# Optimization experiments

Measured on AMD Instinct MI355X. Metric: run time of the kernel, lower is better.

Reference implementation:

```python
import jax, jax.numpy as jnp
import numpy as np

DIM = 128
HEADS = 4
DIM_HEAD = 32
N_EMBD = HEADS * DIM_HEAD  # 128
SCALE = DIM_HEAD ** -0.5


def conv2d(x, w, b):
    # NCHW conv, 3x3, stride 1, SAME padding (= padding=1 in torch)
    out = jax.lax.conv_general_dilated(
        x, w, window_strides=(1, 1), padding='SAME',
        dimension_numbers=('NCHW', 'OIHW', 'NCHW'))
    return out + b[None, :, None, None]


def conv_block(x, w1, b1, w2, b2):
    # Conv -> ReLU -> Conv (the to_q/to_k/to_v pattern)
    return conv2d(jax.nn.relu(conv2d(x, w1, b1)), w2, b2)


def setup_inputs() -> dict:
    key = jax.random.key(0)
    ks = jax.random.split(key, 20)
    B, C, S = 4, DIM, 32
    H, W = 128, 512
    wscale = 0.05

    def cw(k, cout, cin):
        return jax.random.normal(k, (cout, cin, 3, 3), jnp.float32) * wscale

    inp = {
        'x': jax.random.normal(ks[0], (B, C, S, S), jnp.float32),
        'y': jax.random.normal(ks[1], (B, C, H, W), jnp.float32),
        'u': jax.random.randint(ks[2], (B, S, S), 0, W),
        'q_w1': cw(ks[3], N_EMBD, DIM), 'q_b1': jnp.zeros((N_EMBD,), jnp.float32),
        'q_w2': cw(ks[4], N_EMBD, N_EMBD), 'q_b2': jnp.zeros((N_EMBD,), jnp.float32),
        'k_w1': cw(ks[5], N_EMBD, DIM), 'k_b1': jnp.zeros((N_EMBD,), jnp.float32),
        'k_w2': cw(ks[6], N_EMBD, N_EMBD), 'k_b2': jnp.zeros((N_EMBD,), jnp.float32),
        'v_w1': cw(ks[7], N_EMBD, DIM), 'v_b1': jnp.zeros((N_EMBD,), jnp.float32),
        'v_w2': cw(ks[8], N_EMBD, N_EMBD), 'v_b2': jnp.zeros((N_EMBD,), jnp.float32),
        'proj_w': cw(ks[9], DIM, N_EMBD), 'proj_b': jnp.zeros((DIM,), jnp.float32),
    }
    return inp


def reference(x, y, u, q_w1, q_b1, q_w2, q_b2, k_w1, k_b1, k_w2, k_b2,
              v_w1, v_b1, v_w2, v_b2, proj_w, proj_b):
    B, C, S, _ = x.shape
    _, _, H, W = y.shape
    SS = S * S

    # Q from the (B,C,S,S) query grid -> (B, S^2, n_embd)
    q = conv_block(x, q_w1, q_b1, q_w2, q_b2).reshape(B, N_EMBD, SS).transpose(0, 2, 1)

    # K, V from the (B,C,H,W) map
    k = conv_block(y, k_w1, k_b1, k_w2, k_b2)  # (B, E, H, W)
    v = conv_block(y, v_w1, v_b1, v_w2, v_b2)

    # Gather columns of K/V along W per query index u (clamped)
    uc = jnp.clip(u, 0, W - 1).astype(jnp.int32).reshape(B, 1, 1, SS)
    ks = jnp.take_along_axis(k, uc, axis=3).transpose(0, 3, 2, 1)  # (B, SS, H, E)
    vs = jnp.take_along_axis(v, uc, axis=3).transpose(0, 3, 2, 1)  # (B, SS, H, E)

    # Per-query attention over the H axis
    dot = SCALE * jnp.einsum('bqe,bqhe->bqh', q, ks)  # (B, SS, H)
    attn = jax.nn.softmax(dot, axis=-1)
    a = jnp.einsum('bqh,bqhe->bqe', attn, vs)  # (B, SS, E)

    a = a.transpose(0, 2, 1).reshape(B, N_EMBD, S, S)
    z = jax.nn.relu(conv2d(a, proj_w, proj_b))  # (B, DIM, S, S)
    return z
```

## Files before the change

kernel.cpp:

```cpp
#include <hip/hip_runtime.h>
#include <stdint.h>

typedef __attribute__((ext_vector_type(16))) float f32x16;
typedef __attribute__((ext_vector_type(8))) short s16x8;

#define WAITVM(n) asm volatile("s_waitcnt vmcnt(" #n ")" ::: "memory")
#define WAITLGKM0 asm volatile("s_waitcnt lgkmcnt(0)" ::: "memory")

__device__ inline short bf16b(float f) {
  uint32_t x = __float_as_uint(f);
  return (short)((x + 0x7fffu + ((x >> 16) & 1u)) >> 16);
}
__device__ inline float bfu(uint16_t u) { return __uint_as_float(((uint32_t)u) << 16); }

__device__ inline void gll16(const void* g, void* l) {
  __builtin_amdgcn_global_load_lds((const __attribute__((address_space(1))) void*)g,
                                   (__attribute__((address_space(3))) void*)l, 16, 0, 0);
}

__global__ __launch_bounds__(256) void packw_k(
    const float* w0, const float* w1, const float* w2, const float* w3,
    const float* w4, const float* w5, const float* w6, s16x8* dst) {
  const float* srcs[7] = {w0, w1, w2, w3, w4, w5, w6};
  const int widx = blockIdx.y;
  const float* src = srcs[widx];
  const int gid = blockIdx.x * 256 + threadIdx.x;
  const int lane = gid & 63, frag = gid >> 6;
  const int nblk = frag & 3, ks = (frag >> 2) & 1, chunk = (frag >> 3) & 3, tap = frag >> 5;
  const int co = nblk * 32 + (lane & 31);
  const int cib = chunk * 32 + ks * 16 + (lane >> 5) * 8;
  s16x8 v;
#pragma unroll
  for (int j = 0; j < 8; ++j)
    v[j] = bf16b(src[((size_t)co * 128 + cib + j) * 9 + tap]);
  dst[(size_t)widx * 18432 + (size_t)frag * 64 + lane] = v;
}

template <int TW>
__global__ __launch_bounds__(256) void nchw2nhwc_k(
    const float* __restrict__ in, uint16_t* __restrict__ out, int H, int W) {
  __shared__ float tile[128][TW + 1];
  const int b = blockIdx.z, h = blockIdx.y, w0 = blockIdx.x * TW;
  for (int idx = threadIdx.x; idx < 128 * TW; idx += 256) {
    int c = idx / TW, w = idx - c * TW;
    tile[c][w] = in[(((size_t)b * 128 + c) * H + h) * W + w0 + w];
  }
  __syncthreads();
  for (int idx = threadIdx.x; idx < TW * 16; idx += 256) {
    int w = idx >> 4, cg = idx & 15;
    s16x8 v;
#pragma unroll
    for (int j = 0; j < 8; ++j) v[j] = bf16b(tile[cg * 8 + j][w]);
    *reinterpret_cast<s16x8*>(out + ((((size_t)b * H + h) * W + w0 + w) << 7) + cg * 8) = v;
  }
}

template <int OMODE, bool RELU, typename Tout>
__global__ __launch_bounds__(256, 3) void convmf7_k(
    const uint16_t* __restrict__ in, const s16x8* __restrict__ wpk,
    const float* __restrict__ bias, Tout* __restrict__ out,
    const uint16_t* __restrict__ zp, int H, int W) {
  constexpr int CP = 34, RP = 6, RPCP = RP * CP;
  constexpr int SLOTS = 4 * RPCP;
  constexpr int SPT = 4;
  __shared__ s16x8 lds[2][SPT * 256];
  const int b = blockIdx.z, r0 = blockIdx.y * 4, c0 = blockIdx.x * 32;
  const int tid = threadIdx.x, lane = tid & 63, wn = tid >> 6;
  const int wbase = tid & 192;

  const uint16_t* gsrc[SPT];
#pragma unroll
  for (int i = 0; i < SPT; ++i) {
    const int s = tid + i * 256;
    const int kq = s / RPCP;
    const int rem = s - kq * RPCP;
    const int r = rem / CP, c = rem - r * CP;
    const int gr = r0 + r - 1, gc = c0 + c - 1;
    const bool ok = (s < SLOTS) && gr >= 0 && gr < H && gc >= 0 && gc < W;
    gsrc[i] = ok ? (in + (((size_t)b * H + gr) * W + gc) * 128 + kq * 8) : zp;
  }

  const s16x8* __restrict__ wbl = wpk + wn * 64 + lane;
  s16x8 wf[9];
#pragma unroll
  for (int t = 0; t < 9; ++t) wf[t] = wbl[t * 2048];

#pragma unroll
  for (int i = 0; i < SPT; ++i) gll16(gsrc[i], &lds[0][wbase + i * 256]);

  f32x16 acc[4];
#pragma unroll
  for (int i = 0; i < 4; ++i)
#pragma unroll
    for (int r = 0; r < 16; ++r) acc[i][r] = 0.f;

  const int abase = (lane >> 5) * RPCP + (lane & 31);
  WAITVM(0);
  __builtin_amdgcn_s_barrier();
  __builtin_amdgcn_sched_barrier(0);

#pragma unroll
  for (int chunk = 0; chunk < 4; ++chunk) {
    const int cb = chunk & 1;
    const s16x8* __restrict__ Lb = &lds[cb][abase];
#pragma unroll
    for (int p = 0; p < 6; ++p) {
      const int ks = p / 3, kx = p - ks * 3;
      s16x8 ar[6];
#pragma unroll
      for (int r = 0; r < 6; ++r) ar[r] = Lb[ks * 2 * RPCP + r * CP + kx];
      if (chunk < 3 && p < SPT)
        gll16(gsrc[p] + (chunk + 1) * 32, &lds[cb ^ 1][wbase + p * 256]);
      __builtin_amdgcn_sched_barrier(0);
      __builtin_amdgcn_s_barrier();
      WAITLGKM0;
      __builtin_amdgcn_sched_barrier(0);
      __builtin_amdgcn_s_setprio(1);
#pragma unroll
      for (int ky = 0; ky < 3; ++ky) {
#pragma unroll
        for (int mf = 0; mf < 4; ++mf)
          acc[mf] = __builtin_amdgcn_mfma_f32_32x32x16_bf16(ar[mf + ky], wf[ky * 3 + kx],
                                                            acc[mf], 0, 0, 0);
      }
      __builtin_amdgcn_s_setprio(0);
      if (!(chunk == 3 && ks == 1)) {
        const int nc = (ks == 0) ? chunk : chunk + 1;
        const int nks = (ks == 0) ? 1 : 0;
#pragma unroll
        for (int ky = 0; ky < 3; ++ky) {
          const int tap = ky * 3 + kx;
          wf[tap] = wbl[((tap * 4 + nc) * 2 + nks) * 256];
        }
      }
      __builtin_amdgcn_sched_barrier(0);
      if (p == 5 && chunk < 3) WAITVM(9);
      __builtin_amdgcn_s_barrier();
    }
  }

  const int co = wn * 32 + (lane & 31);
  const float bv = bias[co];
#pragma unroll
  for (int mf = 0; mf < 4; ++mf) {
    const int gr = r0 + mf;
#pragma unroll
    for (int reg = 0; reg < 16; ++reg) {
      const int gc = c0 + (reg & 3) + 8 * (reg >> 2) + 4 * (lane >> 5);
      float v = acc[mf][reg] + bv;
      if (RELU) v = fmaxf(v, 0.f);
      size_t idx;
      if (OMODE == 0)      idx = (((size_t)b * H + gr) * W + gc) * 128 + co;
      else if (OMODE == 1) idx = (((size_t)b * W + gc) * H + gr) * 128 + co;
      else                 idx = (((size_t)b * 128 + co) * H + gr) * W + gc;
      if constexpr (sizeof(Tout) == 2) ((uint16_t*)out)[idx] = (uint16_t)bf16b(v);
      else out[idx] = v;
    }
  }
}

__global__ __launch_bounds__(128) void attn_dot_k(
    const float* __restrict__ qg, const uint16_t* __restrict__ Kg,
    const int* __restrict__ u, float* __restrict__ pout) {
  const int bs = blockIdx.x;
  const int b = bs >> 10;
  const int tid = threadIdx.x;
  __shared__ float sq[128];
  __shared__ float wred[2][2];
  sq[tid] = qg[(size_t)bs * 128 + tid];
  int w = u[bs]; w = w < 0 ? 0 : (w > 511 ? 511 : w);
  __syncthreads();
  const s16x8* kp = reinterpret_cast<const s16x8*>(
      Kg + (((size_t)b * 512 + w) * 128 + tid) * 128);
  float acc = 0.f;
#pragma unroll
  for (int i = 0; i < 16; ++i) {
    s16x8 v = kp[i];
#pragma unroll
    for (int j = 0; j < 8; ++j)
      acc = fmaf(sq[i * 8 + j], bfu((uint16_t)v[j]), acc);
  }
  const float d = acc * 0.17677669529663687f;
  float m = d;
#pragma unroll
  for (int o = 1; o < 64; o <<= 1) m = fmaxf(m, __shfl_xor(m, o));
  if ((tid & 63) == 0) wred[0][tid >> 6] = m;
  __syncthreads();
  m = fmaxf(wred[0][0], wred[0][1]);
  const float e = expf(d - m);
  float s = e;
#pragma unroll
  for (int o = 1; o < 64; o <<= 1) s += __shfl_xor(s, o);
  if ((tid & 63) == 0) wred[1][tid >> 6] = s;
  __syncthreads();
  s = wred[1][0] + wred[1][1];
  pout[(size_t)bs * 128 + tid] = e / s;
}

__global__ __launch_bounds__(128) void attn_pv_k(
    const float* __restrict__ pin, const uint16_t* __restrict__ Vg,
    const int* __restrict__ u, uint16_t* __restrict__ aout) {
  const int bs = blockIdx.x;
  const int b = bs >> 10;
  const int tid = threadIdx.x;
  const int eo = tid & 15, hg = tid >> 4;
  __shared__ float sp[128];
  __shared__ float red[8][128];
  sp[tid] = pin[(size_t)bs * 128 + tid];
  int w = u[bs]; w = w < 0 ? 0 : (w > 511 ? 511 : w);
  __syncthreads();
  const s16x8* vp = reinterpret_cast<const s16x8*>(
      Vg + ((size_t)b * 512 + w) * 16384) + eo;
  float a8[8];
#pragma unroll
  for (int j = 0; j < 8; ++j) a8[j] = 0.f;
#pragma unroll
  for (int hh = 0; hh < 16; ++hh) {
    const int h = hg * 16 + hh;
    s16x8 v = vp[h * 16];
    const float p = sp[h];
#pragma unroll
    for (int j = 0; j < 8; ++j) a8[j] = fmaf(p, bfu((uint16_t)v[j]), a8[j]);
  }
#pragma unroll
  for (int j = 0; j < 8; ++j) red[hg][eo * 8 + j] = a8[j];
  __syncthreads();
  float r = 0.f;
#pragma unroll
  for (int g = 0; g < 8; ++g) r += red[g][tid];
  aout[(size_t)bs * 128 + tid] = (uint16_t)bf16b(r);
}

extern "C" void kernel_launch(void* const* d_in, const int* in_sizes, int n_in,
                              void* d_out, int out_size, void* d_ws, size_t ws_size,
                              hipStream_t stream) {
  const float* x      = (const float*)d_in[0];
  const float* y      = (const float*)d_in[1];
  const int*   u      = (const int*)d_in[2];
  const float* q_w1   = (const float*)d_in[3];
  const float* q_b1   = (const float*)d_in[4];
  const float* q_w2   = (const float*)d_in[5];
  const float* q_b2   = (const float*)d_in[6];
  const float* k_w1   = (const float*)d_in[7];
  const float* k_b1   = (const float*)d_in[8];
  const float* k_w2   = (const float*)d_in[9];
  const float* k_b2   = (const float*)d_in[10];
  const float* v_w1   = (const float*)d_in[11];
  const float* v_b1   = (const float*)d_in[12];
  const float* v_w2   = (const float*)d_in[13];
  const float* v_b2   = (const float*)d_in[14];
  const float* proj_w = (const float*)d_in[15];
  const float* proj_b = (const float*)d_in[16];
  float* out = (float*)d_out;

  char* ws = (char*)d_ws;
  const size_t MB = 1 << 20;
  const size_t BIG = 64 * MB;
  const bool tierB = ws_size >= 203 * MB;
  uint16_t* A  = (uint16_t*)ws;
  uint16_t* Bb = (uint16_t*)(ws + BIG);
  uint16_t* KV = tierB ? (uint16_t*)(ws + 2 * BIG) : A;
  char* sm = ws + (tierB ? 3 : 2) * BIG;
  float*    qg  = (float*)sm;
  float*    pb  = (float*)(sm + 2 * MB);
  uint16_t* xbf = (uint16_t*)(sm + 4 * MB);
  uint16_t* t1  = (uint16_t*)(sm + 5 * MB);
  uint16_t* ab  = (uint16_t*)(sm + 6 * MB);
  s16x8*    wpk = (s16x8*)(sm + 7 * MB);
  uint16_t* zp  = (uint16_t*)(sm + 10 * MB);

  hipMemsetAsync(zp, 0, 1024, stream);
  packw_k<<<dim3(72, 7), 256, 0, stream>>>(q_w1, q_w2, k_w1, k_w2, v_w1, v_w2, proj_w, wpk);
  nchw2nhwc_k<32><<<dim3(1, 32, 4), 256, 0, stream>>>(x, xbf, 32, 32);
  nchw2nhwc_k<64><<<dim3(8, 128, 4), 256, 0, stream>>>(y, A, 128, 512);
  convmf7_k<0, true,  uint16_t><<<dim3(1, 8, 4), 256, 0, stream>>>(xbf, wpk + 0 * 18432, q_b1, t1, zp, 32, 32);
  convmf7_k<0, false, float   ><<<dim3(1, 8, 4), 256, 0, stream>>>(t1,  wpk + 1 * 18432, q_b2, qg, zp, 32, 32);
  convmf7_k<0, true,  uint16_t><<<dim3(16, 32, 4), 256, 0, stream>>>(A,  wpk + 2 * 18432, k_b1, Bb, zp, 128, 512);
  convmf7_k<1, false, uint16_t><<<dim3(16, 32, 4), 256, 0, stream>>>(Bb, wpk + 3 * 18432, k_b2, KV, zp, 128, 512);
  attn_dot_k<<<dim3(4096), 128, 0, stream>>>(qg, KV, u, pb);
  if (!tierB) nchw2nhwc_k<64><<<dim3(8, 128, 4), 256, 0, stream>>>(y, A, 128, 512);
  convmf7_k<0, true,  uint16_t><<<dim3(16, 32, 4), 256, 0, stream>>>(A,  wpk + 4 * 18432, v_b1, Bb, zp, 128, 512);
  convmf7_k<1, false, uint16_t><<<dim3(16, 32, 4), 256, 0, stream>>>(Bb, wpk + 5 * 18432, v_b2, KV, zp, 128, 512);
  attn_pv_k<<<dim3(4096), 128, 0, stream>>>(pb, KV, u, ab);
  convmf7_k<3, true, float><<<dim3(1, 8, 4), 256, 0, stream>>>(ab, wpk + 6 * 18432, proj_b, out, zp, 32, 32);
}
```

Measured before the change: 430.8 us.

## Fuse K and V first-layer convolutions into one dual-output MFMA kernel

Adds a conv kernel that loads each input tile of the y feature map into LDS once and computes both the K and V first 3x3 convs, with two accumulator sets and two weight register sets. This halves the input reads and LDS staging for the large first-layer convs and removes one kernel launch. The cost is doubled accumulator and weight register pressure (launch bounds 256,2), which may lower occupancy. It also needs a third big workspace buffer, so the non-fused path is kept for small workspaces.

```diff
diff --git a/kernel.cpp b/kernel.cpp
--- a/kernel.cpp
+++ b/kernel.cpp
@@ -155,6 +155,111 @@
       else                 idx = (((size_t)b * 128 + co) * H + gr) * W + gc;
       if constexpr (sizeof(Tout) == 2) ((uint16_t*)out)[idx] = (uint16_t)bf16b(v);
       else out[idx] = v;
+    }
+  }
+}
+
+__global__ __launch_bounds__(256, 2) void convmf7d_k(
+    const uint16_t* __restrict__ in, const s16x8* __restrict__ wpkK,
+    const s16x8* __restrict__ wpkV, const float* __restrict__ biasK,
+    const float* __restrict__ biasV, uint16_t* __restrict__ outK,
+    uint16_t* __restrict__ outV, const uint16_t* __restrict__ zp, int H, int W) {
+  constexpr int CP = 34, RP = 6, RPCP = RP * CP;
+  constexpr int SLOTS = 4 * RPCP;
+  constexpr int SPT = 4;
+  __shared__ s16x8 lds[2][SPT * 256];
+  const int b = blockIdx.z, r0 = blockIdx.y * 4, c0 = blockIdx.x * 32;
+  const int tid = threadIdx.x, lane = tid & 63, wn = tid >> 6;
+  const int wbase = tid & 192;
+
+  const uint16_t* gsrc[SPT];
+#pragma unroll
+  for (int i = 0; i < SPT; ++i) {
+    const int s = tid + i * 256;
+    const int kq = s / RPCP;
+    const int rem = s - kq * RPCP;
+    const int r = rem / CP, c = rem - r * CP;
+    const int gr = r0 + r - 1, gc = c0 + c - 1;
+    const bool ok = (s < SLOTS) && gr >= 0 && gr < H && gc >= 0 && gc < W;
+    gsrc[i] = ok ? (in + (((size_t)b * H + gr) * W + gc) * 128 + kq * 8) : zp;
+  }
+
+  const s16x8* __restrict__ wblK = wpkK + wn * 64 + lane;
+  const s16x8* __restrict__ wblV = wpkV + wn * 64 + lane;
+  s16x8 wfK[9], wfV[9];
+#pragma unroll
+  for (int t = 0; t < 9; ++t) { wfK[t] = wblK[t * 2048]; wfV[t] = wblV[t * 2048]; }
+
+#pragma unroll
+  for (int i = 0; i < SPT; ++i) gll16(gsrc[i], &lds[0][wbase + i * 256]);
+
+  f32x16 accK[4], accV[4];
+#pragma unroll
+  for (int i = 0; i < 4; ++i)
+#pragma unroll
+    for (int r = 0; r < 16; ++r) { accK[i][r] = 0.f; accV[i][r] = 0.f; }
+
+  const int abase = (lane >> 5) * RPCP + (lane & 31);
+  WAITVM(0);
+  __builtin_amdgcn_s_barrier();
+  __builtin_amdgcn_sched_barrier(0);
+
+#pragma unroll
+  for (int chunk = 0; chunk < 4; ++chunk) {
+    const int cb = chunk & 1;
+    const s16x8* __restrict__ Lb = &lds[cb][abase];
+#pragma unroll
+    for (int p = 0; p < 6; ++p) {
+      const int ks = p / 3, kx = p - ks * 3;
+      s16x8 ar[6];
+#pragma unroll
+      for (int r = 0; r < 6; ++r) ar[r] = Lb[ks * 2 * RPCP + r * CP + kx];
+      if (chunk < 3 && p < SPT)
+        gll16(gsrc[p] + (chunk + 1) * 32, &lds[cb ^ 1][wbase + p * 256]);
+      __builtin_amdgcn_sched_barrier(0);
+      __builtin_amdgcn_s_barrier();
+      WAITLGKM0;
+      __builtin_amdgcn_sched_barrier(0);
+      __builtin_amdgcn_s_setprio(1);
+#pragma unroll
+      for (int ky = 0; ky < 3; ++ky) {
+#pragma unroll
+        for (int mf = 0; mf < 4; ++mf) {
+          accK[mf] = __builtin_amdgcn_mfma_f32_32x32x16_bf16(ar[mf + ky], wfK[ky * 3 + kx],
+                                                             accK[mf], 0, 0, 0);
+          accV[mf] = __builtin_amdgcn_mfma_f32_32x32x16_bf16(ar[mf + ky], wfV[ky * 3 + kx],
+                                                             accV[mf], 0, 0, 0);
+        }
+      }
+      __builtin_amdgcn_s_setprio(0);
+      if (!(chunk == 3 && ks == 1)) {
+        const int nc = (ks == 0) ? chunk : chunk + 1;
+        const int nks = (ks == 0) ? 1 : 0;
+#pragma unroll
+        for (int ky = 0; ky < 3; ++ky) {
+          const int tap = ky * 3 + kx;
+          const int off = ((tap * 4 + nc) * 2 + nks) * 256;
+          wfK[tap] = wblK[off];
+          wfV[tap] = wblV[off];
+        }
+      }
+      __builtin_amdgcn_sched_barrier(0);
+      if (p == 5 && chunk < 3) WAITVM(18);
+      __builtin_amdgcn_s_barrier();
+    }
+  }
+
+  const int co = wn * 32 + (lane & 31);
+  const float bvK = biasK[co], bvV = biasV[co];
+#pragma unroll
+  for (int mf = 0; mf < 4; ++mf) {
+    const int gr = r0 + mf;
+#pragma unroll
+    for (int reg = 0; reg < 16; ++reg) {
+      const int gc = c0 + (reg & 3) + 8 * (reg >> 2) + 4 * (lane >> 5);
+      const size_t idx = (((size_t)b * H + gr) * W + gc) * 128 + co;
+      outK[idx] = (uint16_t)bf16b(fmaxf(accK[mf][reg] + bvK, 0.f));
+      outV[idx] = (uint16_t)bf16b(fmaxf(accV[mf][reg] + bvV, 0.f));
     }
   }
 }
@@ -256,11 +361,11 @@
   char* ws = (char*)d_ws;
   const size_t MB = 1 << 20;
   const size_t BIG = 64 * MB;
-  const bool tierB = ws_size >= 203 * MB;
+  const bool fuse = ws_size >= 203 * MB;
   uint16_t* A  = (uint16_t*)ws;
   uint16_t* Bb = (uint16_t*)(ws + BIG);
-  uint16_t* KV = tierB ? (uint16_t*)(ws + 2 * BIG) : A;
-  char* sm = ws + (tierB ? 3 : 2) * BIG;
+  uint16_t* Cc = (uint16_t*)(ws + 2 * BIG);
+  char* sm = ws + (fuse ? 3 : 2) * BIG;
   float*    qg  = (float*)sm;
   float*    pb  = (float*)(sm + 2 * MB);
   uint16_t* xbf = (uint16_t*)(sm + 4 * MB);
@@ -275,12 +380,22 @@
   nchw2nhwc_k<64><<<dim3(8, 128, 4), 256, 0, stream>>>(y, A, 128, 512);
   convmf7_k<0, true,  uint16_t><<<dim3(1, 8, 4), 256, 0, stream>>>(xbf, wpk + 0 * 18432, q_b1, t1, zp, 32, 32);
   convmf7_k<0, false, float   ><<<dim3(1, 8, 4), 256, 0, stream>>>(t1,  wpk + 1 * 18432, q_b2, qg, zp, 32, 32);
-  convmf7_k<0, true,  uint16_t><<<dim3(16, 32, 4), 256, 0, stream>>>(A,  wpk + 2 * 18432, k_b1, Bb, zp, 128, 512);
-  convmf7_k<1, false, uint16_t><<<dim3(16, 32, 4), 256, 0, stream>>>(Bb, wpk + 3 * 18432, k_b2, KV, zp, 128, 512);
-  attn_dot_k<<<dim3(4096), 128, 0, stream>>>(qg, KV, u, pb);
-  if (!tierB) nchw2nhwc_k<64><<<dim3(8, 128, 4), 256, 0, stream>>>(y, A, 128, 512);
-  convmf7_k<0, true,  uint16_t><<<dim3(16, 32, 4), 256, 0, stream>>>(A,  wpk + 4 * 18432, v_b1, Bb, zp, 128, 512);
-  convmf7_k<1, false, uint16_t><<<dim3(16, 32, 4), 256, 0, stream>>>(Bb, wpk + 5 * 18432, v_b2, KV, zp, 128, 512);
-  attn_pv_k<<<dim3(4096), 128, 0, stream>>>(pb, KV, u, ab);
+
+  if (fuse) {
+    convmf7d_k<<<dim3(16, 32, 4), 256, 0, stream>>>(A, wpk + 2 * 18432, wpk + 4 * 18432,
+                                                    k_b1, v_b1, Bb, Cc, zp, 128, 512);
+    convmf7_k<1, false, uint16_t><<<dim3(16, 32, 4), 256, 0, stream>>>(Bb, wpk + 3 * 18432, k_b2, A, zp, 128, 512);
+    attn_dot_k<<<dim3(4096), 128, 0, stream>>>(qg, A, u, pb);
+    convmf7_k<1, false, uint16_t><<<dim3(16, 32, 4), 256, 0, stream>>>(Cc, wpk + 5 * 18432, v_b2, Bb, zp, 128, 512);
+    attn_pv_k<<<dim3(4096), 128, 0, stream>>>(pb, Bb, u, ab);
+  } else {
+    convmf7_k<0, true,  uint16_t><<<dim3(16, 32, 4), 256, 0, stream>>>(A,  wpk + 2 * 18432, k_b1, Bb, zp, 128, 512);
+    convmf7_k<1, false, uint16_t><<<dim3(16, 32, 4), 256, 0, stream>>>(Bb, wpk + 3 * 18432, k_b2, A, zp, 128, 512);
+    attn_dot_k<<<dim3(4096), 128, 0, stream>>>(qg, A, u, pb);
+    nchw2nhwc_k<64><<<dim3(8, 128, 4), 256, 0, stream>>>(y, A, 128, 512);
+    convmf7_k<0, true,  uint16_t><<<dim3(16, 32, 4), 256, 0, stream>>>(A,  wpk + 4 * 18432, v_b1, Bb, zp, 128, 512);
+    convmf7_k<1, false, uint16_t><<<dim3(16, 32, 4), 256, 0, stream>>>(Bb, wpk + 5 * 18432, v_b2, A, zp, 128, 512);
+    attn_pv_k<<<dim3(4096), 128, 0, stream>>>(pb, A, u, ab);
+  }
   convmf7_k<3, true, float><<<dim3(1, 8, 4), 256, 0, stream>>>(ab, wpk + 6 * 18432, proj_b, out, zp, 32, 32);
 }
```

Result: slower. 442.9 us (+2.8%).
